# Kernel tuning notes

Hardware: AMD Instinct MI355X
Metric: run time of the kernel (lower is better)

## Reference

```python
import jax, jax.numpy as jnp
import numpy as np

PK_ROWS, PK_COLS = 256, 256
BATCH = 32
LSTM = 16
NEIGH = 8  # 8-neighborhood; input_size = NEIGH + 1
DYN_OUT = 1


def _build_grid_edges(rows, cols):
    """Replicates KernelNetwork.__init__ adjacency construction.
    Returns (pos0, coming_from, going_to) int arrays over directed grid edges.
    Direction codes 0..7: TL, T, TR, L, R, BL, B, BR (direction_dict - 1)."""
    offsets = [(-1, -1), (-1, 0), (-1, 1), (0, -1), (0, 1), (1, -1), (1, 0), (1, 1)]
    pos0, coming_from, going_to = [], [], []
    for r in range(rows):
        for c in range(cols):
            pid = r * cols + c
            for d, (dr, dc) in enumerate(offsets):
                nr, nc = r + dr, c + dc
                if 0 <= nr < rows and 0 <= nc < cols:
                    pos0.append(pid)
                    coming_from.append(nr * cols + nc)
                    going_to.append(d)
    return (np.asarray(pos0, np.int64), np.asarray(coming_from, np.int64),
            np.asarray(going_to, np.int64))


def setup_inputs() -> dict:
    key = jax.random.key(0)
    ks = jax.random.split(key, 10)
    P = PK_ROWS * PK_COLS
    pos0, coming_from, going_to = _build_grid_edges(PK_ROWS, PK_COLS)
    s = 0.1  # weight scale
    return {
        "dyn_in": jax.random.normal(ks[0], (BATCH, P), jnp.float32),
        "pk_lat_in": jax.random.normal(ks[1], (BATCH, P, NEIGH), jnp.float32),
        "pk_lat_out": jax.random.normal(ks[2], (BATCH, P, NEIGH), jnp.float32),
        "h": jax.random.normal(ks[3], (BATCH, P, LSTM), jnp.float32),
        "c": jax.random.normal(ks[4], (BATCH, P, LSTM), jnp.float32),
        "Wx": jax.random.normal(ks[5], (NEIGH + 1, 4 * LSTM), jnp.float32) * s,
        "Wh": jax.random.normal(ks[6], (LSTM, 4 * LSTM), jnp.float32) * s,
        "b": jnp.zeros((4 * LSTM,), jnp.float32),
        "Wo": jax.random.normal(ks[7], (LSTM, DYN_OUT + NEIGH), jnp.float32) * s,
        "bo": jnp.zeros((DYN_OUT + NEIGH,), jnp.float32),
        "pos0": jnp.asarray(pos0),
        "coming_from": jnp.asarray(coming_from),
        "going_to": jnp.asarray(going_to),
    }


def reference(dyn_in, pk_lat_in, pk_lat_out, h, c, Wx, Wh, b, Wo, bo,
              pos0, coming_from, going_to):
    # 1) lateral scatter-gather: route each PK's lateral output channel to the
    #    matching neighbor's lateral input slot (irregular gather + scatter).
    lat_in = pk_lat_in.at[:, pos0, going_to].set(
        pk_lat_out[:, coming_from, going_to])  # [B, P, 8]
    # 2) concat dynamic input channel with lateral inputs -> [B, P, 9]
    x = jnp.concatenate([dyn_in[:, :, None], lat_in], axis=2)
    # 3) parallel LSTM cell shared across all PKs
    gates = x @ Wx + h @ Wh + b  # [B, P, 4L]
    i, f, g, o = jnp.split(gates, 4, axis=-1)
    i, f, o = jax.nn.sigmoid(i), jax.nn.sigmoid(f), jax.nn.sigmoid(o)
    g = jnp.tanh(g)
    c_new = f * c + i * g
    h_new = o * jnp.tanh(c_new)
    # 4) output head -> [B, P, dyn_out + 8]; split into dynamic / lateral parts
    out = jnp.tanh(h_new @ Wo + bo)
    pk_dyn_out = out[:, :, :DYN_OUT]
    pk_lat_out_new = out[:, :, DYN_OUT:]
    return pk_dyn_out, pk_lat_out_new, h_new, c_new
```

## Files before the change

kernel.cpp:

```cpp
#include <hip/hip_runtime.h>

#define ROWS 256
#define COLS 256
#define NP (ROWS*COLS)
#define BATCH 32

#define WX_OFF 0
#define WH_OFF 576
#define B_OFF  1600
#define WO_OFF 1664
#define BO_OFF 1808
#define FLAG_OFF 1824

#define OUT_DYN 0
#define OUT_LAT 2097152
#define OUT_H   18874368
#define OUT_C   52428800

using u16 = unsigned short;
using u32 = unsigned int;

__device__ __forceinline__ float bf2f(u16 v){ return __uint_as_float(((u32)v) << 16); }
__device__ __forceinline__ u16 f2bf(float f){
    u32 u = __float_as_uint(f);
    return (u16)((u + 0x7fffu + ((u >> 16) & 1u)) >> 16);
}
__device__ __forceinline__ float rcpf_(float x){ return __builtin_amdgcn_rcpf(x); }
__device__ __forceinline__ float sigm(float x){ return rcpf_(1.f + __expf(-x)); }
__device__ __forceinline__ float tanh_(float x){ return 1.f - 2.f * rcpf_(1.f + __expf(2.f * x)); }
__device__ __forceinline__ void unpack2(u32 u, float& a, float& b){
    a = __uint_as_float(u << 16);
    b = __uint_as_float(u & 0xffff0000u);
}
__device__ __forceinline__ u32 pk2(float a, float b){
    return (u32)f2bf(a) | ((u32)f2bf(b) << 16);
}

__global__ void prep_weights(const void* __restrict__ Wx, const void* __restrict__ Wh,
                             const void* __restrict__ b,  const void* __restrict__ Wo,
                             const void* __restrict__ bo, float* __restrict__ ws){
    __shared__ int sflag;
    const int t = threadIdx.x;
    if (t == 0) sflag = 0;
    __syncthreads();
    float v = bf2f(((const u16*)Wx)[t]);
    if (!(fabsf(v) < 64.0f)) atomicOr(&sflag, 1);
    __syncthreads();
    const int f32in = sflag;

    for (int i = t; i < 576;  i += 256) ws[WX_OFF+i] = f32in ? ((const float*)Wx)[i] : bf2f(((const u16*)Wx)[i]);
    for (int i = t; i < 1024; i += 256) ws[WH_OFF+i] = f32in ? ((const float*)Wh)[i] : bf2f(((const u16*)Wh)[i]);
    for (int i = t; i < 64;   i += 256) ws[B_OFF+i]  = f32in ? ((const float*)b)[i]  : bf2f(((const u16*)b)[i]);
    for (int i = t; i < 144;  i += 256) ws[WO_OFF+i] = f32in ? ((const float*)Wo)[i] : bf2f(((const u16*)Wo)[i]);
    for (int i = t; i < 9;    i += 256) ws[BO_OFF+i] = f32in ? ((const float*)bo)[i] : bf2f(((const u16*)bo)[i]);
    if (t == 0) ((int*)ws)[FLAG_OFF] = f32in;
}

__global__ __launch_bounds__(256) void lstm_step(
    const void* __restrict__ dyn_in,
    const void* __restrict__ lat_in,
    const void* __restrict__ lat_out,
    const void* __restrict__ h_in,
    const void* __restrict__ c_in,
    const float* __restrict__ W,
    void* __restrict__ out)
{
    const int wg = blockIdx.y * gridDim.x + blockIdx.x;
    const int sw = (wg & 7) * ((ROWS * BATCH) / 8) + (wg >> 3);
    const int r   = sw & (ROWS - 1);
    const int bb  = sw >> 8;
    const int col = threadIdx.x;
    const long base = (long)bb * NP + (long)r * COLS + col;
    const int f32in = ((const int*)W)[FLAG_OFF];

    __shared__ float lds[8][3][COLS];

    const int drr[8] = {-1,-1,-1, 0, 0, 1, 1, 1};
    const int dcc[8] = {-1, 0, 1,-1, 1,-1, 0, 1};

    if (f32in){
        #pragma unroll
        for (int rr = 0; rr < 3; rr++){
            int row = r + rr - 1;
            if (row >= 0 && row < ROWS){
                const float4* s = (const float4*)((const float*)lat_out + ((long)bb * NP + (long)row * COLS) * 8);
                float4 a = s[2*col], b4 = s[2*col+1];
                lds[0][rr][col] = a.x;  lds[1][rr][col] = a.y;
                lds[2][rr][col] = a.z;  lds[3][rr][col] = a.w;
                lds[4][rr][col] = b4.x; lds[5][rr][col] = b4.y;
                lds[6][rr][col] = b4.z; lds[7][rr][col] = b4.w;
            }
        }
    } else {
        #pragma unroll
        for (int rr = 0; rr < 3; rr++){
            int row = r + rr - 1;
            if (row >= 0 && row < ROWS){
                const uint4* s = (const uint4*)((const u16*)lat_out + ((long)bb * NP + (long)row * COLS) * 8);
                uint4 a = s[col];
                float e0,e1,e2,e3,e4,e5,e6,e7;
                unpack2(a.x, e0, e1); unpack2(a.y, e2, e3);
                unpack2(a.z, e4, e5); unpack2(a.w, e6, e7);
                lds[0][rr][col] = e0; lds[1][rr][col] = e1;
                lds[2][rr][col] = e2; lds[3][rr][col] = e3;
                lds[4][rr][col] = e4; lds[5][rr][col] = e5;
                lds[6][rr][col] = e6; lds[7][rr][col] = e7;
            }
        }
    }

    float x[9], hv[16];
    if (f32in){
        x[0] = ((const float*)dyn_in)[base];
        const float4* hp = (const float4*)h_in + base * 4;
        #pragma unroll
        for (int qq = 0; qq < 4; qq++){
            float4 hq = hp[qq];
            hv[4*qq+0]=hq.x; hv[4*qq+1]=hq.y; hv[4*qq+2]=hq.z; hv[4*qq+3]=hq.w;
        }
    } else {
        x[0] = bf2f(((const u16*)dyn_in)[base]);
        const uint4* hp = (const uint4*)h_in + base * 2;
        uint4 h0 = hp[0], h1 = hp[1];
        unpack2(h0.x, hv[0], hv[1]);   unpack2(h0.y, hv[2], hv[3]);
        unpack2(h0.z, hv[4], hv[5]);   unpack2(h0.w, hv[6], hv[7]);
        unpack2(h1.x, hv[8], hv[9]);   unpack2(h1.y, hv[10], hv[11]);
        unpack2(h1.z, hv[12], hv[13]); unpack2(h1.w, hv[14], hv[15]);
    }

    __syncthreads();

    #pragma unroll
    for (int d = 0; d < 8; d++){
        int nr = r + drr[d], nc = col + dcc[d];
        if (nr >= 0 && nr < ROWS && nc >= 0 && nc < COLS){
            x[1 + d] = lds[d][drr[d] + 1][nc];
        } else {
            x[1 + d] = f32in ? ((const float*)lat_in)[base * 8 + d]
                             : bf2f(((const u16*)lat_in)[base * 8 + d]);
        }
    }

    float oacc[9];
    #pragma unroll
    for (int t = 0; t < 9; t++) oacc[t] = W[BO_OFF + t];

    #pragma unroll 1
    for (int q = 0; q < 4; q++){
        const int cb = 4 * q;

        float cva, cvb, cvc, cvd;
        if (f32in){
            float4 cq = ((const float4*)c_in)[base * 4 + q];
            cva = cq.x; cvb = cq.y; cvc = cq.z; cvd = cq.w;
        } else {
            uint2 cu = ((const uint2*)c_in)[base * 4 + q];
            unpack2(cu.x, cva, cvb); unpack2(cu.y, cvc, cvd);
        }

        float ai[4], af[4], ag[4], ao[4];
        #pragma unroll
        for (int kk = 0; kk < 4; kk++){
            ai[kk] = W[B_OFF + cb + kk];
            af[kk] = W[B_OFF + 16 + cb + kk];
            ag[kk] = W[B_OFF + 32 + cb + kk];
            ao[kk] = W[B_OFF + 48 + cb + kk];
        }
        #pragma unroll
        for (int m = 0; m < 9; m++){
            const float xm = x[m];
            const float* wb = W + WX_OFF + m * 64 + cb;
            #pragma unroll
            for (int kk = 0; kk < 4; kk++){
                ai[kk] = fmaf(xm, wb[kk],      ai[kk]);
                af[kk] = fmaf(xm, wb[16 + kk], af[kk]);
                ag[kk] = fmaf(xm, wb[32 + kk], ag[kk]);
                ao[kk] = fmaf(xm, wb[48 + kk], ao[kk]);
            }
        }
        #pragma unroll
        for (int m = 0; m < 16; m++){
            const float hm = hv[m];
            const float* wb = W + WH_OFF + m * 64 + cb;
            #pragma unroll
            for (int kk = 0; kk < 4; kk++){
                ai[kk] = fmaf(hm, wb[kk],      ai[kk]);
                af[kk] = fmaf(hm, wb[16 + kk], af[kk]);
                ag[kk] = fmaf(hm, wb[32 + kk], ag[kk]);
                ao[kk] = fmaf(hm, wb[48 + kk], ao[kk]);
            }
        }

        const float cvv[4] = {cva, cvb, cvc, cvd};
        float hn4[4], cn4[4];
        #pragma unroll
        for (int kk = 0; kk < 4; kk++){
            float ig = sigm(ai[kk]);
            float fg = sigm(af[kk]);
            float gg = tanh_(ag[kk]);
            float og = sigm(ao[kk]);
            float cc = fmaf(fg, cvv[kk], ig * gg);
            float hh = og * tanh_(cc);
            cn4[kk] = cc; hn4[kk] = hh;
            const float* wo = W + WO_OFF + (cb + kk) * 9;
            #pragma unroll
            for (int t = 0; t < 9; t++) oacc[t] = fmaf(hh, wo[t], oacc[t]);
        }

        if (f32in){
            float* of = (float*)out;
            ((float4*)(of + OUT_H))[base * 4 + q] = make_float4(hn4[0], hn4[1], hn4[2], hn4[3]);
            ((float4*)(of + OUT_C))[base * 4 + q] = make_float4(cn4[0], cn4[1], cn4[2], cn4[3]);
        } else {
            u16* ob = (u16*)out;
            ((uint2*)(ob + OUT_H))[base * 4 + q] = make_uint2(pk2(hn4[0], hn4[1]), pk2(hn4[2], hn4[3]));
            ((uint2*)(ob + OUT_C))[base * 4 + q] = make_uint2(pk2(cn4[0], cn4[1]), pk2(cn4[2], cn4[3]));
        }
    }

    float dynout = tanh_(oacc[0]);
    float ov[8];
    #pragma unroll
    for (int t = 0; t < 8; t++) ov[t] = tanh_(oacc[1 + t]);

    if (f32in){
        float* of = (float*)out;
        of[OUT_DYN + base] = dynout;
        float4* lp = (float4*)(of + OUT_LAT) + base * 2;
        lp[0] = make_float4(ov[0], ov[1], ov[2], ov[3]);
        lp[1] = make_float4(ov[4], ov[5], ov[6], ov[7]);
    } else {
        u16* ob = (u16*)out;
        ob[OUT_DYN + base] = f2bf(dynout);
        *((uint4*)(ob + OUT_LAT) + base) =
            make_uint4(pk2(ov[0], ov[1]), pk2(ov[2], ov[3]), pk2(ov[4], ov[5]), pk2(ov[6], ov[7]));
    }
}

extern "C" void kernel_launch(void* const* d_in, const int* in_sizes, int n_in,
                              void* d_out, int out_size, void* d_ws, size_t ws_size,
                              hipStream_t stream){
    const void* dyn  = d_in[0];
    const void* lin  = d_in[1];
    const void* lout = d_in[2];
    const void* h    = d_in[3];
    const void* c    = d_in[4];
    const void* Wx   = d_in[5];
    const void* Wh   = d_in[6];
    const void* b    = d_in[7];
    const void* Wo   = d_in[8];
    const void* bo   = d_in[9];
    float* ws = (float*)d_ws;

    hipLaunchKernelGGL(prep_weights, dim3(1), dim3(256), 0, stream, Wx, Wh, b, Wo, bo, ws);
    hipLaunchKernelGGL(lstm_step, dim3(ROWS, BATCH), dim3(256), 0, stream,
                       dyn, lin, lout, h, c, ws, d_out);
}
```

Baseline: 764.9 us.

## Hoist c loads, defer h/c stores, use nontemporal accesses and unroll gate loop

```diff
diff --git a/kernel.cpp b/kernel.cpp
--- a/kernel.cpp
+++ b/kernel.cpp
@@ -19,6 +19,8 @@
 
 using u16 = unsigned short;
 using u32 = unsigned int;
+using f32x4 = __attribute__((ext_vector_type(4))) float;
+using u32x4 = __attribute__((ext_vector_type(4))) u32;
 
 __device__ __forceinline__ float bf2f(u16 v){ return __uint_as_float(((u32)v) << 16); }
 __device__ __forceinline__ u16 f2bf(float f){
@@ -56,7 +58,7 @@
     if (t == 0) ((int*)ws)[FLAG_OFF] = f32in;
 }
 
-__global__ __launch_bounds__(256) void lstm_step(
+__global__ __launch_bounds__(256, 4) void lstm_step(
     const void* __restrict__ dyn_in,
     const void* __restrict__ lat_in,
     const void* __restrict__ lat_out,
@@ -65,7 +67,7 @@
     const float* __restrict__ W,
     void* __restrict__ out)
 {
-    const int wg = blockIdx.y * gridDim.x + blockIdx.x;
+    const int wg = blockIdx.y * (int)gridDim.x + blockIdx.x;
     const int sw = (wg & 7) * ((ROWS * BATCH) / 8) + (wg >> 3);
     const int r   = sw & (ROWS - 1);
     const int bb  = sw >> 8;
@@ -83,8 +85,8 @@
         for (int rr = 0; rr < 3; rr++){
             int row = r + rr - 1;
             if (row >= 0 && row < ROWS){
-                const float4* s = (const float4*)((const float*)lat_out + ((long)bb * NP + (long)row * COLS) * 8);
-                float4 a = s[2*col], b4 = s[2*col+1];
+                const f32x4* s = (const f32x4*)((const float*)lat_out + ((long)bb * NP + (long)row * COLS) * 8);
+                f32x4 a = s[2*col], b4 = s[2*col+1];
                 lds[0][rr][col] = a.x;  lds[1][rr][col] = a.y;
                 lds[2][rr][col] = a.z;  lds[3][rr][col] = a.w;
                 lds[4][rr][col] = b4.x; lds[5][rr][col] = b4.y;
@@ -96,8 +98,8 @@
         for (int rr = 0; rr < 3; rr++){
             int row = r + rr - 1;
             if (row >= 0 && row < ROWS){
-                const uint4* s = (const uint4*)((const u16*)lat_out + ((long)bb * NP + (long)row * COLS) * 8);
-                uint4 a = s[col];
+                const u32x4* s = (const u32x4*)((const u16*)lat_out + ((long)bb * NP + (long)row * COLS) * 8);
+                u32x4 a = s[col];
                 float e0,e1,e2,e3,e4,e5,e6,e7;
                 unpack2(a.x, e0, e1); unpack2(a.y, e2, e3);
                 unpack2(a.z, e4, e5); unpack2(a.w, e6, e7);
@@ -109,23 +111,34 @@
         }
     }
 
-    float x[9], hv[16];
+    float x[9], hv[16], cv[16];
     if (f32in){
-        x[0] = ((const float*)dyn_in)[base];
-        const float4* hp = (const float4*)h_in + base * 4;
+        x[0] = __builtin_nontemporal_load((const float*)dyn_in + base);
+        const f32x4* hp = (const f32x4*)h_in + base * 4;
+        const f32x4* cp = (const f32x4*)c_in + base * 4;
         #pragma unroll
         for (int qq = 0; qq < 4; qq++){
-            float4 hq = hp[qq];
+            f32x4 hq = __builtin_nontemporal_load(hp + qq);
+            f32x4 cq = __builtin_nontemporal_load(cp + qq);
             hv[4*qq+0]=hq.x; hv[4*qq+1]=hq.y; hv[4*qq+2]=hq.z; hv[4*qq+3]=hq.w;
+            cv[4*qq+0]=cq.x; cv[4*qq+1]=cq.y; cv[4*qq+2]=cq.z; cv[4*qq+3]=cq.w;
         }
     } else {
         x[0] = bf2f(((const u16*)dyn_in)[base]);
-        const uint4* hp = (const uint4*)h_in + base * 2;
-        uint4 h0 = hp[0], h1 = hp[1];
+        const u32x4* hp = (const u32x4*)h_in + base * 2;
+        const u32x4* cp = (const u32x4*)c_in + base * 2;
+        u32x4 h0 = __builtin_nontemporal_load(hp);
+        u32x4 h1 = __builtin_nontemporal_load(hp + 1);
+        u32x4 c0 = __builtin_nontemporal_load(cp);
+        u32x4 c1 = __builtin_nontemporal_load(cp + 1);
         unpack2(h0.x, hv[0], hv[1]);   unpack2(h0.y, hv[2], hv[3]);
         unpack2(h0.z, hv[4], hv[5]);   unpack2(h0.w, hv[6], hv[7]);
         unpack2(h1.x, hv[8], hv[9]);   unpack2(h1.y, hv[10], hv[11]);
         unpack2(h1.z, hv[12], hv[13]); unpack2(h1.w, hv[14], hv[15]);
+        unpack2(c0.x, cv[0], cv[1]);   unpack2(c0.y, cv[2], cv[3]);
+        unpack2(c0.z, cv[4], cv[5]);   unpack2(c0.w, cv[6], cv[7]);
+        unpack2(c1.x, cv[8], cv[9]);   unpack2(c1.y, cv[10], cv[11]);
+        unpack2(c1.z, cv[12], cv[13]); unpack2(c1.w, cv[14], cv[15]);
     }
 
     __syncthreads();
@@ -144,20 +157,11 @@
     float oacc[9];
     #pragma unroll
     for (int t = 0; t < 9; t++) oacc[t] = W[BO_OFF + t];
-
-    #pragma unroll 1
+    float hn[16], cn[16];
+
+    #pragma unroll
     for (int q = 0; q < 4; q++){
         const int cb = 4 * q;
-
-        float cva, cvb, cvc, cvd;
-        if (f32in){
-            float4 cq = ((const float4*)c_in)[base * 4 + q];
-            cva = cq.x; cvb = cq.y; cvc = cq.z; cvd = cq.w;
-        } else {
-            uint2 cu = ((const uint2*)c_in)[base * 4 + q];
-            unpack2(cu.x, cva, cvb); unpack2(cu.y, cvc, cvd);
-        }
-
         float ai[4], af[4], ag[4], ao[4];
         #pragma unroll
         for (int kk = 0; kk < 4; kk++){
@@ -190,32 +194,19 @@
                 ao[kk] = fmaf(hm, wb[48 + kk], ao[kk]);
             }
         }
-
-        const float cvv[4] = {cva, cvb, cvc, cvd};
-        float hn4[4], cn4[4];
         #pragma unroll
         for (int kk = 0; kk < 4; kk++){
             float ig = sigm(ai[kk]);
             float fg = sigm(af[kk]);
             float gg = tanh_(ag[kk]);
             float og = sigm(ao[kk]);
-            float cc = fmaf(fg, cvv[kk], ig * gg);
+            float cc = fmaf(fg, cv[cb + kk], ig * gg);
             float hh = og * tanh_(cc);
-            cn4[kk] = cc; hn4[kk] = hh;
+            cn[cb + kk] = cc; hn[cb + kk] = hh;
             const float* wo = W + WO_OFF + (cb + kk) * 9;
             #pragma unroll
             for (int t = 0; t < 9; t++) oacc[t] = fmaf(hh, wo[t], oacc[t]);
         }
-
-        if (f32in){
-            float* of = (float*)out;
-            ((float4*)(of + OUT_H))[base * 4 + q] = make_float4(hn4[0], hn4[1], hn4[2], hn4[3]);
-            ((float4*)(of + OUT_C))[base * 4 + q] = make_float4(cn4[0], cn4[1], cn4[2], cn4[3]);
-        } else {
-            u16* ob = (u16*)out;
-            ((uint2*)(ob + OUT_H))[base * 4 + q] = make_uint2(pk2(hn4[0], hn4[1]), pk2(hn4[2], hn4[3]));
-            ((uint2*)(ob + OUT_C))[base * 4 + q] = make_uint2(pk2(cn4[0], cn4[1]), pk2(cn4[2], cn4[3]));
-        }
     }
 
     float dynout = tanh_(oacc[0]);
@@ -225,15 +216,33 @@
 
     if (f32in){
         float* of = (float*)out;
-        of[OUT_DYN + base] = dynout;
-        float4* lp = (float4*)(of + OUT_LAT) + base * 2;
-        lp[0] = make_float4(ov[0], ov[1], ov[2], ov[3]);
-        lp[1] = make_float4(ov[4], ov[5], ov[6], ov[7]);
+        __builtin_nontemporal_store(dynout, of + OUT_DYN + base);
+        f32x4* lp = (f32x4*)(of + OUT_LAT) + base * 2;
+        __builtin_nontemporal_store((f32x4){ov[0], ov[1], ov[2], ov[3]}, lp);
+        __builtin_nontemporal_store((f32x4){ov[4], ov[5], ov[6], ov[7]}, lp + 1);
+        f32x4* hp2 = (f32x4*)(of + OUT_H) + base * 4;
+        f32x4* cp2 = (f32x4*)(of + OUT_C) + base * 4;
+        #pragma unroll
+        for (int qq = 0; qq < 4; qq++){
+            __builtin_nontemporal_store((f32x4){hn[4*qq], hn[4*qq+1], hn[4*qq+2], hn[4*qq+3]}, hp2 + qq);
+            __builtin_nontemporal_store((f32x4){cn[4*qq], cn[4*qq+1], cn[4*qq+2], cn[4*qq+3]}, cp2 + qq);
+        }
     } else {
         u16* ob = (u16*)out;
-        ob[OUT_DYN + base] = f2bf(dynout);
-        *((uint4*)(ob + OUT_LAT) + base) =
-            make_uint4(pk2(ov[0], ov[1]), pk2(ov[2], ov[3]), pk2(ov[4], ov[5]), pk2(ov[6], ov[7]));
+        __builtin_nontemporal_store(f2bf(dynout), ob + OUT_DYN + base);
+        __builtin_nontemporal_store((u32x4){pk2(ov[0], ov[1]), pk2(ov[2], ov[3]),
+                                            pk2(ov[4], ov[5]), pk2(ov[6], ov[7])},
+                                    (u32x4*)(ob + OUT_LAT) + base);
+        u32x4* hop = (u32x4*)(ob + OUT_H) + base * 2;
+        u32x4* cop = (u32x4*)(ob + OUT_C) + base * 2;
+        __builtin_nontemporal_store((u32x4){pk2(hn[0], hn[1]), pk2(hn[2], hn[3]),
+                                            pk2(hn[4], hn[5]), pk2(hn[6], hn[7])}, hop);
+        __builtin_nontemporal_store((u32x4){pk2(hn[8], hn[9]), pk2(hn[10], hn[11]),
+                                            pk2(hn[12], hn[13]), pk2(hn[14], hn[15])}, hop + 1);
+        __builtin_nontemporal_store((u32x4){pk2(cn[0], cn[1]), pk2(cn[2], cn[3]),
+                                            pk2(cn[4], cn[5]), pk2(cn[6], cn[7])}, cop);
+        __builtin_nontemporal_store((u32x4){pk2(cn[8], cn[9]), pk2(cn[10], cn[11]),
+                                            pk2(cn[12], cn[13]), pk2(cn[14], cn[15])}, cop + 1);
     }
 }
 
```

Measured after the change: 1.166 ms. 1.52x slower.
